# Optimization experiments

Hardware: AMD Instinct MI355X
Metric: run time of the kernel (lower is better)

The kernel has to match this reference:

```python
import jax, jax.numpy as jnp
import numpy as np

N, E, H = 50000, 800000, 4
IN_C, HID, OUT = 256, 64, 64
NEG_SLOPE = 0.2   # PyG GATConv default leaky_relu slope
EPS_BN = 1e-5
EPS_SM = 1e-16    # PyG softmax denominator eps


def setup_inputs() -> dict:
    key = jax.random.key(0)
    ks = jax.random.split(key, 16)
    inp = {
        "x": jax.random.normal(ks[0], (N, IN_C), jnp.float32),
        "edge_index": jax.random.randint(ks[1], (2, E), 0, N, jnp.int32),
    }
    dims = [(IN_C, HID), (HID, HID), (HID, OUT)]
    j = 2
    for l, (di, do) in enumerate(dims):
        s = 1.0 / np.sqrt(di)
        inp[f"W{l}"] = jax.random.normal(ks[j], (di, H * do), jnp.float32) * s; j += 1
        inp[f"as{l}"] = jax.random.normal(ks[j], (H, do), jnp.float32) * 0.1; j += 1
        inp[f"ad{l}"] = jax.random.normal(ks[j], (H, do), jnp.float32) * 0.1; j += 1
        inp[f"b{l}"] = jnp.zeros((do,), jnp.float32)
    for l in range(2):  # BN after all but the last conv
        inp[f"g{l}"] = jnp.ones((HID,), jnp.float32)
        inp[f"be{l}"] = jnp.zeros((HID,), jnp.float32)
    return inp


def _gat_layer(x, src, dst, W, a_src, a_dst, bias):
    """PyG GATConv, heads=H, concat=False (mean over heads), add_self_loops already in src/dst."""
    n = x.shape[0]
    C = a_src.shape[1]
    h = (x @ W).reshape(n, H, C)                      # [N,H,C]
    a_l = jnp.einsum('nhc,hc->nh', h, a_src)          # src attention term per node
    a_r = jnp.einsum('nhc,hc->nh', h, a_dst)          # dst attention term per node
    e = jax.nn.leaky_relu(a_l[src] + a_r[dst], NEG_SLOPE)   # [E',H]
    # segment softmax over incoming edges of each dst node
    m = jax.ops.segment_max(e, dst, num_segments=n)
    m = jnp.where(jnp.isfinite(m), m, 0.0)
    p = jnp.exp(e - m[dst])
    den = jax.ops.segment_sum(p, dst, num_segments=n)
    alpha = p / (den[dst] + EPS_SM)                   # [E',H]
    msg = h[src] * alpha[:, :, None]                  # [E',H,C]
    out = jax.ops.segment_sum(msg, dst, num_segments=n)
    return out.mean(axis=1) + bias                    # concat=False -> head mean, then bias


def _bn(x, g, b):
    # BatchNorm1d training-mode statistics (biased variance), eps=1e-5
    mu = x.mean(axis=0)
    var = x.var(axis=0)
    return (x - mu) * jax.lax.rsqrt(var + EPS_BN) * g + b


def reference(x, edge_index, W0, as0, ad0, b0, W1, as1, ad1, b1,
              W2, as2, ad2, b2, g0, be0, g1, be1):
    n = x.shape[0]
    loops = jnp.arange(n, dtype=edge_index.dtype)
    src = jnp.concatenate([edge_index[0], loops])
    dst = jnp.concatenate([edge_index[1], loops])

    h = _gat_layer(x, src, dst, W0, as0, ad0, b0)
    h = jax.nn.relu(_bn(h, g0, be0))                  # dropout: eval mode (identity)
    h = _gat_layer(h, src, dst, W1, as1, ad1, b1)
    h = jax.nn.relu(_bn(h, g1, be1))
    out = _gat_layer(h, src, dst, W2, as2, ad2, b2)
    return out
```

## Files before the change

kernel.cpp:

```cpp
#include <hip/hip_runtime.h>
#include <hip/hip_fp16.h>
#include <math.h>

constexpr float NEG_SLOPE = 0.2f;
constexpr float EPS_BN = 1e-5f;
constexpr float EPS_SM = 1e-16f;

typedef _Float16 half8 __attribute__((ext_vector_type(8)));
typedef float f32x4 __attribute__((ext_vector_type(4)));

__device__ __forceinline__ float lrelu(float x){ return x >= 0.f ? x : NEG_SLOPE * x; }

__global__ void k_prep(int* cnt, int n, float* bn, int* tick,
                       const float* __restrict__ W0, const float* __restrict__ W1,
                       const float* __restrict__ W2, _Float16* __restrict__ Wt0,
                       _Float16* __restrict__ Wt1, _Float16* __restrict__ Wt2){
  int t = blockIdx.x * blockDim.x + threadIdx.x;
  if (t < n) cnt[t] = 0;
  if (t < 256) bn[t] = 0.f;
  if (t < 4) tick[t] = 0;
  if (t < 65536){
    int c = t & 255, k = t >> 8;
    Wt0[(size_t)c * 256 + k] = (_Float16)W0[(size_t)k * 256 + c];
  } else if (t < 81920){
    int u = t - 65536; int c = u & 255, k = u >> 8;
    Wt1[(size_t)c * 64 + k] = (_Float16)W1[(size_t)k * 256 + c];
  } else if (t < 98304){
    int u = t - 81920; int c = u & 255, k = u >> 8;
    Wt2[(size_t)c * 64 + k] = (_Float16)W2[(size_t)k * 256 + c];
  }
}

__global__ void k_count(const int* __restrict__ ei, int E, int N, int* __restrict__ cnt){
  int e = blockIdx.x * blockDim.x + threadIdx.x;
  if (e >= E + N) return;
  int dst = (e < E) ? ei[E + e] : (e - E);
  atomicAdd(&cnt[dst], 1);
}

__global__ __launch_bounds__(256) void k_bsumscan(const int* __restrict__ cnt, int n, int chunk,
                                                  int* __restrict__ part, int* __restrict__ ptr,
                                                  int* __restrict__ tick){
  __shared__ int s[256];
  __shared__ int amLast;
  int b = blockIdx.x, t = threadIdx.x;
  int lo = b * chunk, hi = min(n, lo + chunk);
  int v = 0;
  for (int i = lo + t; i < hi; i += 256) v += cnt[i];
  s[t] = v;
  __syncthreads();
  #pragma unroll
  for (int off = 128; off > 0; off >>= 1){
    if (t < off) s[t] += s[t + off];
    __syncthreads();
  }
  if (t == 0) part[b] = s[0];
  __threadfence();
  if (t == 0) amLast = (atomicAdd(tick, 1) == (int)gridDim.x - 1) ? 1 : 0;
  __syncthreads();
  if (amLast){
    int pv = atomicAdd(&part[t], 0);
    s[t] = pv;
    __syncthreads();
    #pragma unroll
    for (int off = 1; off < 256; off <<= 1){
      int u = (t >= off) ? s[t - off] : 0;
      __syncthreads();
      s[t] += u;
      __syncthreads();
    }
    part[t] = s[t] - pv;
    if (t == 255) ptr[n] = s[255];
  }
}

__global__ __launch_bounds__(256) void k_localscan(const int* __restrict__ cnt, const int* __restrict__ part,
                                                   int n, int chunk, int* __restrict__ ptr,
                                                   int* __restrict__ cursor){
  __shared__ int s[256];
  int b = blockIdx.x, t = threadIdx.x;
  int i = b * chunk + t;
  int v = (t < chunk && i < n) ? cnt[i] : 0;
  s[t] = v;
  __syncthreads();
  #pragma unroll
  for (int off = 1; off < 256; off <<= 1){
    int u = (t >= off) ? s[t - off] : 0;
    __syncthreads();
    s[t] += u;
    __syncthreads();
  }
  if (t < chunk && i < n){
    int ex = part[b] + s[t] - v;
    ptr[i] = ex;
    cursor[i] = ex;
  }
}

__global__ void k_fill(const int* __restrict__ ei, int E, int N,
                       int* __restrict__ cursor, int* __restrict__ csr_src){
  int e = blockIdx.x * blockDim.x + threadIdx.x;
  if (e >= E + N) return;
  int src, dst;
  if (e < E){ src = ei[e]; dst = ei[E + e]; } else { src = e - E; dst = e - E; }
  int slot = atomicAdd(&cursor[dst], 1);
  csr_src[slot] = src;
}

__global__ __launch_bounds__(256, 2) void k_gemm(const float* __restrict__ X,
    const _Float16* __restrict__ Wt, const float* __restrict__ a_s, const float* __restrict__ a_d,
    __half* __restrict__ hb, float* __restrict__ al, float* __restrict__ ar, int nrows, int K,
    const float* __restrict__ scale, const float* __restrict__ shift){
  __shared__ _Float16 Alds[4][129][8];
  __shared__ _Float16 Blds[4][257][8];
  int tid = threadIdx.x;
  int m0 = blockIdx.x * 128;
  int w = tid >> 6, l = tid & 63;
  int lm = l & 15, lq = l >> 4;
  int qs = tid & 3, rs = tid >> 2;
  f32x4 acc[8][4] = {};

  for (int k0 = 0; k0 < K; k0 += 32){
    float4 sc0, sc1, sh0, sh1;
    if (scale){
      sc0 = *(const float4*)(scale + k0 + qs * 8);
      sc1 = *(const float4*)(scale + k0 + qs * 8 + 4);
      sh0 = *(const float4*)(shift + k0 + qs * 8);
      sh1 = *(const float4*)(shift + k0 + qs * 8 + 4);
    }
    #pragma unroll
    for (int it = 0; it < 2; it++){
      int row = it * 64 + rs;
      int gr = m0 + row;
      float4 v0 = make_float4(0,0,0,0), v1 = make_float4(0,0,0,0);
      if (gr < nrows){
        v0 = *(const float4*)(X + (size_t)gr * K + k0 + qs * 8);
        v1 = *(const float4*)(X + (size_t)gr * K + k0 + qs * 8 + 4);
      }
      if (scale){
        v0.x = fmaxf(fmaf(v0.x, sc0.x, sh0.x), 0.f);
        v0.y = fmaxf(fmaf(v0.y, sc0.y, sh0.y), 0.f);
        v0.z = fmaxf(fmaf(v0.z, sc0.z, sh0.z), 0.f);
        v0.w = fmaxf(fmaf(v0.w, sc0.w, sh0.w), 0.f);
        v1.x = fmaxf(fmaf(v1.x, sc1.x, sh1.x), 0.f);
        v1.y = fmaxf(fmaf(v1.y, sc1.y, sh1.y), 0.f);
        v1.z = fmaxf(fmaf(v1.z, sc1.z, sh1.z), 0.f);
        v1.w = fmaxf(fmaf(v1.w, sc1.w, sh1.w), 0.f);
      }
      half8 h = {(_Float16)v0.x, (_Float16)v0.y, (_Float16)v0.z, (_Float16)v0.w,
                 (_Float16)v1.x, (_Float16)v1.y, (_Float16)v1.z, (_Float16)v1.w};
      *(half8*)&Alds[qs][row][0] = h;
    }
    #pragma unroll
    for (int it = 0; it < 4; it++){
      int col = it * 64 + rs;
      *(half8*)&Blds[qs][col][0] = *(const half8*)(Wt + (size_t)col * K + k0 + qs * 8);
    }
    __syncthreads();
    half8 af[8];
    #pragma unroll
    for (int mf = 0; mf < 8; mf++) af[mf] = *(const half8*)&Alds[lq][mf * 16 + lm][0];
    #pragma unroll
    for (int j = 0; j < 4; j++){
      half8 bf = *(const half8*)&Blds[lq][(w * 4 + j) * 16 + lm][0];
      #pragma unroll
      for (int mf = 0; mf < 8; mf++)
        acc[mf][j] = __builtin_amdgcn_mfma_f32_16x16x32_f16(af[mf], bf, acc[mf][j], 0, 0, 0);
    }
    __syncthreads();
  }

  float asv[4], adv[4];
  #pragma unroll
  for (int j = 0; j < 4; j++){
    asv[j] = a_s[w * 64 + j * 16 + lm];
    adv[j] = a_d[w * 64 + j * 16 + lm];
  }
  #pragma unroll
  for (int mf = 0; mf < 8; mf++){
    #pragma unroll
    for (int reg = 0; reg < 4; reg++){
      float sl = acc[mf][0][reg] * asv[0] + acc[mf][1][reg] * asv[1]
               + acc[mf][2][reg] * asv[2] + acc[mf][3][reg] * asv[3];
      float sr = acc[mf][0][reg] * adv[0] + acc[mf][1][reg] * adv[1]
               + acc[mf][2][reg] * adv[2] + acc[mf][3][reg] * adv[3];
      #pragma unroll
      for (int off = 1; off < 16; off <<= 1){
        sl += __shfl_xor(sl, off);
        sr += __shfl_xor(sr, off);
      }
      int row = m0 + mf * 16 + lq * 4 + reg;
      if (lm == 0 && row < nrows){
        al[(size_t)row * 4 + w] = sl;
        ar[(size_t)row * 4 + w] = sr;
      }
    }
    #pragma unroll
    for (int j = 0; j < 4; j++){
      #pragma unroll
      for (int reg = 0; reg < 4; reg++){
        int row = m0 + mf * 16 + lq * 4 + reg;
        if (row < nrows)
          hb[(size_t)row * 256 + w * 64 + j * 16 + lm] = __float2half(acc[mf][j][reg]);
      }
    }
  }
}

__global__ __launch_bounds__(256) void k_node(const int* __restrict__ ptr,
    const int* __restrict__ csr, const __half* __restrict__ hb,
    const float* __restrict__ al, const float* __restrict__ ar,
    const float* __restrict__ bias, float* __restrict__ out, int N){
  __shared__ int2 ssw[4][64][4];
  int n = (blockIdx.x * blockDim.x + threadIdx.x) >> 6;
  int lane = threadIdx.x & 63;
  int wv = threadIdx.x >> 6;
  if (n >= N) return;
  int beg = ptr[n], end = ptr[n + 1];
  int deg = end - beg;
  float4 arv = *(const float4*)(ar + (size_t)n * 4);
  int hd = lane >> 4;
  int cg = (lane & 15) * 4;
  const __half* hbase = hb + hd * 64 + cg;
  float ax = 0.f, ay = 0.f, az = 0.f, aw = 0.f;

  if (deg <= 64){
    int idx = beg + lane;
    bool act = idx < end;
    int mye = act ? csr[idx] : 0;
    float e0 = -1e30f, e1 = -1e30f, e2 = -1e30f, e3 = -1e30f;
    if (act){
      float4 av = *(const float4*)(al + (size_t)mye * 4);
      e0 = lrelu(av.x + arv.x); e1 = lrelu(av.y + arv.y);
      e2 = lrelu(av.z + arv.z); e3 = lrelu(av.w + arv.w);
    }
    float m0 = e0, m1 = e1, m2 = e2, m3 = e3;
    #pragma unroll
    for (int off = 32; off > 0; off >>= 1){
      m0 = fmaxf(m0, __shfl_xor(m0, off));
      m1 = fmaxf(m1, __shfl_xor(m1, off));
      m2 = fmaxf(m2, __shfl_xor(m2, off));
      m3 = fmaxf(m3, __shfl_xor(m3, off));
    }
    float w0 = __expf(e0 - m0), w1 = __expf(e1 - m1);
    float w2 = __expf(e2 - m2), w3 = __expf(e3 - m3);
    float d0 = w0, d1 = w1, d2 = w2, d3 = w3;
    #pragma unroll
    for (int off = 32; off > 0; off >>= 1){
      d0 += __shfl_xor(d0, off);
      d1 += __shfl_xor(d1, off);
      d2 += __shfl_xor(d2, off);
      d3 += __shfl_xor(d3, off);
    }
    int4* wr = (int4*)&ssw[wv][lane][0];
    wr[0] = make_int4(mye, __float_as_int(w0 / (d0 + EPS_SM)),
                      mye, __float_as_int(w1 / (d1 + EPS_SM)));
    wr[1] = make_int4(mye, __float_as_int(w2 / (d2 + EPS_SM)),
                      mye, __float_as_int(w3 / (d3 + EPS_SM)));
    __builtin_amdgcn_wave_barrier();
    const int2* phd = &ssw[wv][0][hd];
    #pragma unroll 4
    for (int j = 0; j < deg; j++){
      int2 sw = phd[j * 4];
      float w = __int_as_float(sw.y);
      ushort4 u = *(const ushort4*)(hbase + (size_t)sw.x * 256);
      ax = fmaf(__half2float(__ushort_as_half(u.x)), w, ax);
      ay = fmaf(__half2float(__ushort_as_half(u.y)), w, ay);
      az = fmaf(__half2float(__ushort_as_half(u.z)), w, az);
      aw = fmaf(__half2float(__ushort_as_half(u.w)), w, aw);
    }
  } else {
    float m0 = -1e30f, m1 = -1e30f, m2 = -1e30f, m3 = -1e30f;
    for (int i = beg + lane; i < end; i += 64){
      int s = csr[i];
      float4 av = *(const float4*)(al + (size_t)s * 4);
      m0 = fmaxf(m0, lrelu(av.x + arv.x));
      m1 = fmaxf(m1, lrelu(av.y + arv.y));
      m2 = fmaxf(m2, lrelu(av.z + arv.z));
      m3 = fmaxf(m3, lrelu(av.w + arv.w));
    }
    #pragma unroll
    for (int off = 32; off > 0; off >>= 1){
      m0 = fmaxf(m0, __shfl_xor(m0, off));
      m1 = fmaxf(m1, __shfl_xor(m1, off));
      m2 = fmaxf(m2, __shfl_xor(m2, off));
      m3 = fmaxf(m3, __shfl_xor(m3, off));
    }
    float d0 = 0.f, d1 = 0.f, d2 = 0.f, d3 = 0.f;
    for (int i = beg + lane; i < end; i += 64){
      int s = csr[i];
      float4 av = *(const float4*)(al + (size_t)s * 4);
      d0 += __expf(lrelu(av.x + arv.x) - m0);
      d1 += __expf(lrelu(av.y + arv.y) - m1);
      d2 += __expf(lrelu(av.z + arv.z) - m2);
      d3 += __expf(lrelu(av.w + arv.w) - m3);
    }
    #pragma unroll
    for (int off = 32; off > 0; off >>= 1){
      d0 += __shfl_xor(d0, off);
      d1 += __shfl_xor(d1, off);
      d2 += __shfl_xor(d2, off);
      d3 += __shfl_xor(d3, off);
    }
    float i0 = 1.f / (d0 + EPS_SM), i1 = 1.f / (d1 + EPS_SM);
    float i2 = 1.f / (d2 + EPS_SM), i3 = 1.f / (d3 + EPS_SM);
    float arh = hd == 0 ? arv.x : hd == 1 ? arv.y : hd == 2 ? arv.z : arv.w;
    float mh  = hd == 0 ? m0 : hd == 1 ? m1 : hd == 2 ? m2 : m3;
    float ih  = hd == 0 ? i0 : hd == 1 ? i1 : hd == 2 ? i2 : i3;
    for (int i = beg; i < end; i++){
      int s = csr[i];
      float w = __expf(lrelu(al[(size_t)s * 4 + hd] + arh) - mh) * ih;
      ushort4 u = *(const ushort4*)(hbase + (size_t)s * 256);
      ax = fmaf(__half2float(__ushort_as_half(u.x)), w, ax);
      ay = fmaf(__half2float(__ushort_as_half(u.y)), w, ay);
      az = fmaf(__half2float(__ushort_as_half(u.z)), w, az);
      aw = fmaf(__half2float(__ushort_as_half(u.w)), w, aw);
    }
  }

  #pragma unroll
  for (int off = 16; off <= 32; off <<= 1){
    ax += __shfl_xor(ax, off);
    ay += __shfl_xor(ay, off);
    az += __shfl_xor(az, off);
    aw += __shfl_xor(aw, off);
  }
  if (lane < 16){
    float4 b4 = *(const float4*)(bias + cg);
    *(float4*)(out + (size_t)n * 64 + cg) =
        make_float4(ax * 0.25f + b4.x, ay * 0.25f + b4.y, az * 0.25f + b4.z, aw * 0.25f + b4.w);
  }
}

__global__ __launch_bounds__(256) void k_bnstats(const float* __restrict__ x, int N,
                                                 float* __restrict__ gsum, float* __restrict__ gsq,
                                                 int* __restrict__ tick,
                                                 const float* __restrict__ g, const float* __restrict__ be,
                                                 float* __restrict__ scale, float* __restrict__ shift){
  int c = threadIdx.x & 63;
  int rg = threadIdx.x >> 6;
  float s = 0.f, q = 0.f;
  for (int r = blockIdx.x * 4 + rg; r < N; r += gridDim.x * 4){
    float v = x[(size_t)r * 64 + c];
    s += v; q += v * v;
  }
  __shared__ float ls[4][64], lq[4][64];
  __shared__ int amLast;
  ls[rg][c] = s; lq[rg][c] = q;
  __syncthreads();
  if (rg == 0){
    s = ls[0][c] + ls[1][c] + ls[2][c] + ls[3][c];
    q = lq[0][c] + lq[1][c] + lq[2][c] + lq[3][c];
    atomicAdd(&gsum[c], s);
    atomicAdd(&gsq[c], q);
  }
  __threadfence();
  if (threadIdx.x == 0)
    amLast = (atomicAdd(tick, 1) == (int)gridDim.x - 1) ? 1 : 0;
  __syncthreads();
  if (amLast && threadIdx.x < 64){
    float gs = atomicAdd(&gsum[c], 0.f);
    float gq = atomicAdd(&gsq[c], 0.f);
    float m = gs / (float)N;
    float v = gq / (float)N - m * m;
    float sc = g[c] * rsqrtf(v + EPS_BN);
    scale[c] = sc;
    shift[c] = be[c] - m * sc;
  }
}

extern "C" void kernel_launch(void* const* d_in, const int* in_sizes, int n_in,
                              void* d_out, int out_size, void* d_ws, size_t ws_size,
                              hipStream_t stream){
  const float* x  = (const float*)d_in[0];
  const int*   ei = (const int*)d_in[1];
  const float* W[3]  = {(const float*)d_in[2], (const float*)d_in[6],  (const float*)d_in[10]};
  const float* AS[3] = {(const float*)d_in[3], (const float*)d_in[7],  (const float*)d_in[11]};
  const float* AD[3] = {(const float*)d_in[4], (const float*)d_in[8],  (const float*)d_in[12]};
  const float* BI[3] = {(const float*)d_in[5], (const float*)d_in[9],  (const float*)d_in[13]};
  const float* G[2]  = {(const float*)d_in[14], (const float*)d_in[16]};
  const float* BE[2] = {(const float*)d_in[15], (const float*)d_in[17]};
  const int N = in_sizes[0] / 256;
  const int E = in_sizes[1] / 2;
  const int EN = E + N;

  char* wsb = (char*)d_ws;
  size_t off = 0;
  auto alloc = [&](size_t bytes) -> char* {
    char* p = wsb + off;
    off = (off + bytes + 255) & ~(size_t)255;
    return p;
  };
  int* cnt      = (int*)alloc((size_t)N * 4);
  int* cursor   = (int*)alloc((size_t)N * 4);
  int* rowptr   = (int*)alloc((size_t)(N + 1) * 4);
  int* part     = (int*)alloc(256 * 4);
  int* csr      = (int*)alloc((size_t)EN * 4);
  _Float16* Wt0 = (_Float16*)alloc((size_t)256 * 256 * 2);
  _Float16* Wt1 = (_Float16*)alloc((size_t)64 * 256 * 2);
  _Float16* Wt2 = (_Float16*)alloc((size_t)64 * 256 * 2);
  __half* hb    = (__half*)alloc((size_t)N * 256 * 2);
  float* al     = (float*)alloc((size_t)N * 4 * 4);
  float* ar     = (float*)alloc((size_t)N * 4 * 4);
  float* bufA   = (float*)alloc((size_t)N * 64 * 4);
  float* bn     = (float*)alloc(256 * 4);
  int*   tick   = (int*)alloc(4 * 4);
  float* murs   = (float*)alloc(128 * 4);

  const int chunk = (N + 255) / 256;

  k_prep<<<384, 256, 0, stream>>>(cnt, N, bn, tick, W[0], W[1], W[2], Wt0, Wt1, Wt2);
  k_count<<<(EN + 255) / 256, 256, 0, stream>>>(ei, E, N, cnt);
  k_bsumscan<<<256, 256, 0, stream>>>(cnt, N, chunk, part, rowptr, tick + 2);
  k_localscan<<<256, 256, 0, stream>>>(cnt, part, N, chunk, rowptr, cursor);
  k_fill<<<(EN + 255) / 256, 256, 0, stream>>>(ei, E, N, cursor, csr);

  const _Float16* Wt[3] = {Wt0, Wt1, Wt2};
  const float* lin = x;
  for (int l = 0; l < 3; l++){
    int K = (l == 0) ? 256 : 64;
    const float* sc = (l == 0) ? nullptr : murs;
    const float* sh = (l == 0) ? nullptr : murs + 64;
    k_gemm<<<(N + 127) / 128, 256, 0, stream>>>(lin, Wt[l], AS[l], AD[l], hb, al, ar, N, K, sc, sh);
    float* outp = (l == 2) ? (float*)d_out : bufA;
    k_node<<<(N + 3) / 4, 256, 0, stream>>>(rowptr, csr, hb, al, ar, BI[l], outp, N);
    if (l < 2){
      float* gsum = bn + l * 128;
      float* gsq  = gsum + 64;
      k_bnstats<<<128, 256, 0, stream>>>(bufA, N, gsum, gsq, tick + l, G[l], BE[l], murs, murs + 64);
      lin = bufA;
    }
  }
}
```

Measured before the change: 559.3 us.

## Widen node gather to 16-byte loads and place self loops directly in CSR

The aggregation loop for low-degree nodes now has each lane load 8 halves (16 bytes) of a source row and handle two edges per step across the wave halves, with a final cross-lane reduction. Softmax weights and source indices are kept in separate shared arrays. Self loops are no longer counted and filled with atomics: counts start at 1 and the local scan writes each node's self loop into the last slot of its segment. The aim is fewer gather instructions and fewer atomics, at the cost of a wider shuffle reduction and a possible out-of-range shared read when the degree is odd.

```diff
diff --git a/kernel.cpp b/kernel.cpp
--- a/kernel.cpp
+++ b/kernel.cpp
@@ -16,7 +16,7 @@
                        const float* __restrict__ W2, _Float16* __restrict__ Wt0,
                        _Float16* __restrict__ Wt1, _Float16* __restrict__ Wt2){
   int t = blockIdx.x * blockDim.x + threadIdx.x;
-  if (t < n) cnt[t] = 0;
+  if (t < n) cnt[t] = 1;
   if (t < 256) bn[t] = 0.f;
   if (t < 4) tick[t] = 0;
   if (t < 65536){
@@ -31,11 +31,10 @@
   }
 }
 
-__global__ void k_count(const int* __restrict__ ei, int E, int N, int* __restrict__ cnt){
+__global__ void k_count(const int* __restrict__ ei, int E, int* __restrict__ cnt){
   int e = blockIdx.x * blockDim.x + threadIdx.x;
-  if (e >= E + N) return;
-  int dst = (e < E) ? ei[E + e] : (e - E);
-  atomicAdd(&cnt[dst], 1);
+  if (e >= E) return;
+  atomicAdd(&cnt[ei[E + e]], 1);
 }
 
 __global__ __launch_bounds__(256) void k_bsumscan(const int* __restrict__ cnt, int n, int chunk,
@@ -76,7 +75,7 @@
 
 __global__ __launch_bounds__(256) void k_localscan(const int* __restrict__ cnt, const int* __restrict__ part,
                                                    int n, int chunk, int* __restrict__ ptr,
-                                                   int* __restrict__ cursor){
+                                                   int* __restrict__ cursor, int* __restrict__ csr_src){
   __shared__ int s[256];
   int b = blockIdx.x, t = threadIdx.x;
   int i = b * chunk + t;
@@ -94,15 +93,15 @@
     int ex = part[b] + s[t] - v;
     ptr[i] = ex;
     cursor[i] = ex;
-  }
-}
-
-__global__ void k_fill(const int* __restrict__ ei, int E, int N,
+    csr_src[ex + v - 1] = i;
+  }
+}
+
+__global__ void k_fill(const int* __restrict__ ei, int E,
                        int* __restrict__ cursor, int* __restrict__ csr_src){
   int e = blockIdx.x * blockDim.x + threadIdx.x;
-  if (e >= E + N) return;
-  int src, dst;
-  if (e < E){ src = ei[e]; dst = ei[E + e]; } else { src = e - E; dst = e - E; }
+  if (e >= E) return;
+  int src = ei[e], dst = ei[E + e];
   int slot = atomicAdd(&cursor[dst], 1);
   csr_src[slot] = src;
 }
@@ -211,7 +210,8 @@
     const int* __restrict__ csr, const __half* __restrict__ hb,
     const float* __restrict__ al, const float* __restrict__ ar,
     const float* __restrict__ bias, float* __restrict__ out, int N){
-  __shared__ int2 ssw[4][64][4];
+  __shared__ float4 wsm[4][64];
+  __shared__ int    ssm[4][64];
   int n = (blockIdx.x * blockDim.x + threadIdx.x) >> 6;
   int lane = threadIdx.x & 63;
   int wv = threadIdx.x >> 6;
@@ -219,10 +219,6 @@
   int beg = ptr[n], end = ptr[n + 1];
   int deg = end - beg;
   float4 arv = *(const float4*)(ar + (size_t)n * 4);
-  int hd = lane >> 4;
-  int cg = (lane & 15) * 4;
-  const __half* hbase = hb + hd * 64 + cg;
-  float ax = 0.f, ay = 0.f, az = 0.f, aw = 0.f;
 
   if (deg <= 64){
     int idx = beg + lane;
@@ -230,7 +226,7 @@
     int mye = act ? csr[idx] : 0;
     float e0 = -1e30f, e1 = -1e30f, e2 = -1e30f, e3 = -1e30f;
     if (act){
-      float4 av = *(const float4*)(al + (size_t)mye * 4);
+      float4 av = *(const float4*)((const char*)al + ((unsigned)mye << 4));
       e0 = lrelu(av.x + arv.x); e1 = lrelu(av.y + arv.y);
       e2 = lrelu(av.z + arv.z); e3 = lrelu(av.w + arv.w);
     }
@@ -252,24 +248,52 @@
       d2 += __shfl_xor(d2, off);
       d3 += __shfl_xor(d3, off);
     }
-    int4* wr = (int4*)&ssw[wv][lane][0];
-    wr[0] = make_int4(mye, __float_as_int(w0 / (d0 + EPS_SM)),
-                      mye, __float_as_int(w1 / (d1 + EPS_SM)));
-    wr[1] = make_int4(mye, __float_as_int(w2 / (d2 + EPS_SM)),
-                      mye, __float_as_int(w3 / (d3 + EPS_SM)));
+    wsm[wv][lane] = make_float4(w0 / (d0 + EPS_SM), w1 / (d1 + EPS_SM),
+                                w2 / (d2 + EPS_SM), w3 / (d3 + EPS_SM));
+    ssm[wv][lane] = mye;
     __builtin_amdgcn_wave_barrier();
-    const int2* phd = &ssw[wv][0][hd];
-    #pragma unroll 4
-    for (int j = 0; j < deg; j++){
-      int2 sw = phd[j * 4];
-      float w = __int_as_float(sw.y);
-      ushort4 u = *(const ushort4*)(hbase + (size_t)sw.x * 256);
-      ax = fmaf(__half2float(__ushort_as_half(u.x)), w, ax);
-      ay = fmaf(__half2float(__ushort_as_half(u.y)), w, ay);
-      az = fmaf(__half2float(__ushort_as_half(u.z)), w, az);
-      aw = fmaf(__half2float(__ushort_as_half(u.w)), w, aw);
+
+    int eh = lane >> 5;
+    int hd = (lane >> 3) & 3;
+    int c8 = lane & 7;
+    unsigned choff = (unsigned)(hd * 128 + c8 * 16);
+    const float* wbase = (const float*)&wsm[wv][0];
+    float a0=0.f,a1=0.f,a2=0.f,a3=0.f,a4=0.f,a5=0.f,a6=0.f,a7=0.f;
+    #pragma unroll 2
+    for (int j = 0; j < deg; j += 2){
+      int je = j + eh;
+      int s = ssm[wv][je];
+      float w = wbase[je * 4 + hd];
+      int4 q = *(const int4*)((const char*)hb + (((unsigned)s << 9) + choff));
+      const __half2* h2 = (const __half2*)&q;
+      float2 f0 = __half22float2(h2[0]);
+      float2 f1 = __half22float2(h2[1]);
+      float2 f2 = __half22float2(h2[2]);
+      float2 f3 = __half22float2(h2[3]);
+      a0 = fmaf(f0.x, w, a0); a1 = fmaf(f0.y, w, a1);
+      a2 = fmaf(f1.x, w, a2); a3 = fmaf(f1.y, w, a3);
+      a4 = fmaf(f2.x, w, a4); a5 = fmaf(f2.y, w, a5);
+      a6 = fmaf(f3.x, w, a6); a7 = fmaf(f3.y, w, a7);
+    }
+    #pragma unroll
+    for (int off = 32; off >= 8; off >>= 1){
+      a0 += __shfl_xor(a0, off); a1 += __shfl_xor(a1, off);
+      a2 += __shfl_xor(a2, off); a3 += __shfl_xor(a3, off);
+      a4 += __shfl_xor(a4, off); a5 += __shfl_xor(a5, off);
+      a6 += __shfl_xor(a6, off); a7 += __shfl_xor(a7, off);
+    }
+    if (lane < 8){
+      float* op = out + (size_t)n * 64 + c8 * 8;
+      float4 b0 = *(const float4*)(bias + c8 * 8);
+      float4 b1 = *(const float4*)(bias + c8 * 8 + 4);
+      *(float4*)op       = make_float4(a0*0.25f+b0.x, a1*0.25f+b0.y, a2*0.25f+b0.z, a3*0.25f+b0.w);
+      *(float4*)(op + 4) = make_float4(a4*0.25f+b1.x, a5*0.25f+b1.y, a6*0.25f+b1.z, a7*0.25f+b1.w);
     }
   } else {
+    int hd = lane >> 4;
+    int cg = (lane & 15) * 4;
+    const __half* hbase = hb + hd * 64 + cg;
+    float ax = 0.f, ay = 0.f, az = 0.f, aw = 0.f;
     float m0 = -1e30f, m1 = -1e30f, m2 = -1e30f, m3 = -1e30f;
     for (int i = beg + lane; i < end; i += 64){
       int s = csr[i];
@@ -316,19 +340,18 @@
       az = fmaf(__half2float(__ushort_as_half(u.z)), w, az);
       aw = fmaf(__half2float(__ushort_as_half(u.w)), w, aw);
     }
-  }
-
-  #pragma unroll
-  for (int off = 16; off <= 32; off <<= 1){
-    ax += __shfl_xor(ax, off);
-    ay += __shfl_xor(ay, off);
-    az += __shfl_xor(az, off);
-    aw += __shfl_xor(aw, off);
-  }
-  if (lane < 16){
-    float4 b4 = *(const float4*)(bias + cg);
-    *(float4*)(out + (size_t)n * 64 + cg) =
-        make_float4(ax * 0.25f + b4.x, ay * 0.25f + b4.y, az * 0.25f + b4.z, aw * 0.25f + b4.w);
+    #pragma unroll
+    for (int off = 16; off <= 32; off <<= 1){
+      ax += __shfl_xor(ax, off);
+      ay += __shfl_xor(ay, off);
+      az += __shfl_xor(az, off);
+      aw += __shfl_xor(aw, off);
+    }
+    if (lane < 16){
+      float4 b4 = *(const float4*)(bias + cg);
+      *(float4*)(out + (size_t)n * 64 + cg) =
+          make_float4(ax * 0.25f + b4.x, ay * 0.25f + b4.y, az * 0.25f + b4.z, aw * 0.25f + b4.w);
+    }
   }
 }
 
@@ -410,10 +433,10 @@
   const int chunk = (N + 255) / 256;
 
   k_prep<<<384, 256, 0, stream>>>(cnt, N, bn, tick, W[0], W[1], W[2], Wt0, Wt1, Wt2);
-  k_count<<<(EN + 255) / 256, 256, 0, stream>>>(ei, E, N, cnt);
+  k_count<<<(E + 255) / 256, 256, 0, stream>>>(ei, E, cnt);
   k_bsumscan<<<256, 256, 0, stream>>>(cnt, N, chunk, part, rowptr, tick + 2);
-  k_localscan<<<256, 256, 0, stream>>>(cnt, part, N, chunk, rowptr, cursor);
-  k_fill<<<(EN + 255) / 256, 256, 0, stream>>>(ei, E, N, cursor, csr);
+  k_localscan<<<256, 256, 0, stream>>>(cnt, part, N, chunk, rowptr, cursor, csr);
+  k_fill<<<(E + 255) / 256, 256, 0, stream>>>(ei, E, cursor, csr);
 
   const _Float16* Wt[3] = {Wt0, Wt1, Wt2};
   const float* lin = x;
```

Result: no change. 565.8 us (+1.2%).
